# Optimization experiments

Hardware: AMD Instinct MI355X
Metric: run time of the kernel (lower is better)

The kernel has to match this reference:

```python
import jax, jax.numpy as jnp
import numpy as np

BT, H, V = 4096, 2048, 32000
BETA = 0.5
TEMPERATURE = 1.0
W_SCALE = 0.02  # keep logits in a sane range so softmax is not saturated


def setup_inputs() -> dict:
    key = jax.random.key(0)
    k1, k2, k3, k4 = jax.random.split(key, 4)
    return {
        "student_input": jax.random.normal(k1, (BT, H), dtype=jnp.float32),
        "teacher_input": jax.random.normal(k2, (BT, H), dtype=jnp.float32),
        "w_student": jax.random.normal(k3, (V, H), dtype=jnp.float32) * W_SCALE,
        "w_teacher": jax.random.normal(k4, (V, H), dtype=jnp.float32) * W_SCALE,
    }


def reference(student_input, teacher_input, w_student, w_teacher):
    # Fused linear + generalized Jensen-Shannon divergence (Liger semantics).
    # logits = x @ W.T, temperature-scaled before softmax.
    s_logits = jnp.einsum("nh,vh->nv", student_input, w_student) / TEMPERATURE
    t_logits = jnp.einsum("nh,vh->nv", teacher_input, w_teacher) / TEMPERATURE
    log_q = jax.nn.log_softmax(s_logits, axis=-1)  # student
    log_p = jax.nn.log_softmax(t_logits, axis=-1)  # teacher
    p = jnp.exp(log_p)
    q = jnp.exp(log_q)
    m = BETA * p + (1.0 - BETA) * q
    log_m = jnp.log(m)
    # JSD_beta(P || Q) = beta*KL(P||M) + (1-beta)*KL(Q||M), mean over tokens
    loss = BETA * jnp.sum(p * (log_p - log_m)) + (1.0 - BETA) * jnp.sum(q * (log_q - log_m))
    return loss / BT
```

## Files before the change

kernel.cpp:

```cpp
#include <hip/hip_runtime.h>
#include <cstdint>

#define BT 4096
#define HD 2048
#define VD 32000

typedef __attribute__((ext_vector_type(4))) float float4_t;
typedef __attribute__((ext_vector_type(4))) short short4_t;
typedef __attribute__((ext_vector_type(8))) short short8_t;
typedef __attribute__((ext_vector_type(8))) unsigned short ushort8_t;

constexpr int BM = 128, BN = 128, BK = 32;

__device__ __forceinline__ unsigned short f2bf(float f) {
  unsigned u = __float_as_uint(f);
  u += 0x7FFFu + ((u >> 16) & 1u);
  return (unsigned short)(u >> 16);
}

__device__ __forceinline__ float bf2f(unsigned short h) {
  return __uint_as_float((unsigned)h << 16);
}

__device__ __forceinline__ short8_t pack8(float4_t a, float4_t b) {
  short8_t h;
  h[0] = (short)f2bf(a.x); h[1] = (short)f2bf(a.y);
  h[2] = (short)f2bf(a.z); h[3] = (short)f2bf(a.w);
  h[4] = (short)f2bf(b.x); h[5] = (short)f2bf(b.y);
  h[6] = (short)f2bf(b.z); h[7] = (short)f2bf(b.w);
  return h;
}

__device__ __forceinline__ void async_copy16(const void* g, void* l) {
  __builtin_amdgcn_global_load_lds(
      (__attribute__((address_space(1))) void*)(uintptr_t)(g),
      (__attribute__((address_space(3))) void*)(uint32_t)(uintptr_t)(l),
      16, 0, 0);
}

__global__ __launch_bounds__(256) void cast_f32_to_bf16(
    const float4_t* __restrict__ in, short4_t* __restrict__ out, int n4) {
  for (int i = blockIdx.x * 256 + threadIdx.x; i < n4; i += gridDim.x * 256) {
    float4_t v = in[i];
    short4_t o;
    o.x = (short)f2bf(v.x); o.y = (short)f2bf(v.y);
    o.z = (short)f2bf(v.z); o.w = (short)f2bf(v.w);
    out[i] = o;
  }
}

__global__ __launch_bounds__(256) void cast_all_fp8(
    const float4_t* __restrict__ xs, const float4_t* __restrict__ xt,
    const float4_t* __restrict__ ws, const float4_t* __restrict__ wt,
    unsigned int* __restrict__ oxs, unsigned int* __restrict__ oxt,
    unsigned int* __restrict__ ows, unsigned int* __restrict__ owt,
    float* __restrict__ out) {
  const long XN4 = (long)BT * HD / 4;
  const long WN4 = (long)VD * HD / 4;
  const long total = 2 * (XN4 + WN4);
  const long i0 = blockIdx.x * 256L + threadIdx.x;
  if (i0 == 0) out[0] = 0.6931471805599453f;
  for (long i = i0; i < total; i += gridDim.x * 256L) {
    const float4_t* s; unsigned int* d; float scl; long j = i;
    if (j < XN4) { s = xs; d = oxs; scl = 1.f; }
    else if ((j -= XN4) < XN4) { s = xt; d = oxt; scl = 1.f; }
    else if ((j -= XN4) < WN4) { s = ws; d = ows; scl = 64.f; }
    else { j -= WN4; s = wt; d = owt; scl = 64.f; }
    float4_t v = s[j];
    int p = __builtin_amdgcn_cvt_pk_fp8_f32(v.x * scl, v.y * scl, 0, false);
    p = __builtin_amdgcn_cvt_pk_fp8_f32(v.z * scl, v.w * scl, p, true);
    d[j] = (unsigned int)p;
  }
}

__device__ __forceinline__ int swz(int row) { return (row ^ (row >> 2)) & 3; }

template <bool F32SRC>
__device__ __forceinline__ void ktile(const void* A, const void* B,
                                      float4_t (&acc)[4][4],
                                      unsigned short* As, unsigned short* Bs,
                                      int m0, int n0) {
  const int tid = threadIdx.x;
  const int lane = tid & 63;
  const int wave = tid >> 6;
  const int wm = wave >> 1, wn = wave & 1;
  const int r0 = tid >> 2, c0 = tid & 3;
  const int cg = c0 ^ swz(r0);
  const int row16 = lane & 15, kq = lane >> 4;
  const int kqs = kq ^ swz(row16);
  const int aoff = (wm * 64 + row16) * BK + kqs * 8;
  const int boff = (wn * 64 + row16) * BK + kqs * 8;
  const int lds0 = __builtin_amdgcn_readfirstlane(wave * 1024);
  const int lds1 = __builtin_amdgcn_readfirstlane(4096 + wave * 1024);

  const unsigned short* Ab = nullptr; const unsigned short* Bb = nullptr;
  const float* Af = nullptr; const float* Bf = nullptr;
  if constexpr (!F32SRC) {
    Ab = (const unsigned short*)A + (size_t)(m0 + r0) * HD + cg * 8;
    Bb = (const unsigned short*)B + (size_t)(n0 + r0) * HD + cg * 8;
  } else {
    Af = (const float*)A + (size_t)(m0 + r0) * HD + cg * 8;
    Bf = (const float*)B + (size_t)(n0 + r0) * HD + cg * 8;
  }

  for (int kb = 0; kb < HD / BK; ++kb) {
    const int ke = kb * BK;
    if constexpr (!F32SRC) {
      async_copy16(Ab + ke, (char*)As + lds0);
      async_copy16(Ab + (size_t)64 * HD + ke, (char*)As + lds1);
      async_copy16(Bb + ke, (char*)Bs + lds0);
      async_copy16(Bb + (size_t)64 * HD + ke, (char*)Bs + lds1);
    } else {
      short8_t hA0 = pack8(*(const float4_t*)(Af + ke), *(const float4_t*)(Af + ke + 4));
      short8_t hA1 = pack8(*(const float4_t*)(Af + (size_t)64 * HD + ke),
                           *(const float4_t*)(Af + (size_t)64 * HD + ke + 4));
      short8_t hB0 = pack8(*(const float4_t*)(Bf + ke), *(const float4_t*)(Bf + ke + 4));
      short8_t hB1 = pack8(*(const float4_t*)(Bf + (size_t)64 * HD + ke),
                           *(const float4_t*)(Bf + (size_t)64 * HD + ke + 4));
      *(short8_t*)((char*)As + tid * 16) = hA0;
      *(short8_t*)((char*)As + 4096 + tid * 16) = hA1;
      *(short8_t*)((char*)Bs + tid * 16) = hB0;
      *(short8_t*)((char*)Bs + 4096 + tid * 16) = hB1;
    }
    __syncthreads();
    short8_t af[4], bfv[4];
#pragma unroll
    for (int mi = 0; mi < 4; ++mi) af[mi] = *(const short8_t*)(As + aoff + mi * 16 * BK);
#pragma unroll
    for (int ni = 0; ni < 4; ++ni) bfv[ni] = *(const short8_t*)(Bs + boff + ni * 16 * BK);
#pragma unroll
    for (int mi = 0; mi < 4; ++mi)
#pragma unroll
      for (int ni = 0; ni < 4; ++ni)
        acc[mi][ni] = __builtin_amdgcn_mfma_f32_16x16x32_bf16(af[mi], bfv[ni], acc[mi][ni], 0, 0, 0);
    __syncthreads();
  }
}

template <bool F32SRC, bool STORE>
__global__ __launch_bounds__(256, 2) void gemm_pass1(
    const void* A0, const void* A1, const void* B0, const void* B1,
    float* __restrict__ rowsum, unsigned short* __restrict__ store) {
  __shared__ __align__(16) unsigned short As[BM * BK];
  __shared__ __align__(16) unsigned short Bs[BN * BK];
  const int m0 = blockIdx.x * BM;
  const int n0 = blockIdx.y * BN;
  const int z = blockIdx.z;
  const void* A = z ? A1 : A0;
  const void* B = z ? B1 : B0;
  float4_t acc[4][4] = {};
  ktile<F32SRC>(A, B, acc, As, Bs, m0, n0);

  const int tid = threadIdx.x;
  const int lane = tid & 63;
  const int wave = tid >> 6;
  const int wm = wave >> 1, wn = wave & 1;
  const int row16 = lane & 15, kq = lane >> 4;

  if constexpr (STORE) {
    unsigned short* st = store + (size_t)z * BT * VD;
#pragma unroll
    for (int mi = 0; mi < 4; ++mi)
#pragma unroll
      for (int r = 0; r < 4; ++r) {
        const size_t grow = (size_t)(m0 + wm * 64 + mi * 16 + kq * 4 + r);
        const size_t gc0 = (size_t)(n0 + wn * 64 + row16);
#pragma unroll
        for (int ni = 0; ni < 4; ++ni)
          st[grow * VD + gc0 + ni * 16] = f2bf(acc[mi][ni][r]);
      }
  }

  float* rs = rowsum + z * BT;
#pragma unroll
  for (int mi = 0; mi < 4; ++mi)
#pragma unroll
    for (int r = 0; r < 4; ++r) {
      float s = __expf(acc[mi][0][r]) + __expf(acc[mi][1][r]) +
                __expf(acc[mi][2][r]) + __expf(acc[mi][3][r]);
      s += __shfl_xor(s, 1);
      s += __shfl_xor(s, 2);
      s += __shfl_xor(s, 4);
      s += __shfl_xor(s, 8);
      if (row16 == 0) atomicAdd(&rs[m0 + wm * 64 + mi * 16 + kq * 4 + r], s);
    }
}

constexpr int NKT8 = HD / 64;

__global__ __launch_bounds__(512, 2) void gemm256_fp8_pass1(
    const unsigned char* __restrict__ fXs, const unsigned char* __restrict__ fXt,
    const unsigned char* __restrict__ fWs, const unsigned char* __restrict__ fWt,
    float* __restrict__ rowsum, unsigned short* __restrict__ store) {
  __shared__ __align__(16) unsigned char lds8[4 * 32768];

  const int z = blockIdx.y;
  const unsigned char* A = z ? fXt : fXs;
  const unsigned char* B = z ? fWt : fWs;

  const int o = blockIdx.x;
  const int s = (o & 7) * 250 + (o >> 3);
  const int m0 = (s & 15) * 256;
  const int n0 = (s >> 4) * 256;

  const int tid = threadIdx.x;
  const int lane = tid & 63;
  const int wave = tid >> 6;
  const int wm = wave >> 2;
  const int wn = wave & 3;
  const int row16 = lane & 15, kq = lane >> 4;
  const int rh = row16 >> 1;
  const int slot = row16 & 1;
  const int cA8 = (((slot << 2) | (kq >> 1)) ^ rh);

  const int lr = lane >> 3, lc = lane & 7;
  const int cl = lc ^ lr;
  const int k16 = (cl & 3) * 16;
  const int mloc0 = (wave * 2 + 0) * 16 + 2 * lr + (cl >> 2);
  const int mloc1 = (wave * 2 + 1) * 16 + 2 * lr + (cl >> 2);
  const unsigned char* srcA0 = A + (size_t)(m0 + mloc0) * HD + k16;
  const unsigned char* srcA1 = A + (size_t)(m0 + mloc1) * HD + k16;
  const unsigned char* srcB0 = B + (size_t)(n0 + mloc0) * HD + k16;
  const unsigned char* srcB1 = B + (size_t)(n0 + mloc1) * HD + k16;
  const int stA0 = __builtin_amdgcn_readfirstlane((wave * 2 + 0) * 1024);
  const int stA1 = __builtin_amdgcn_readfirstlane((wave * 2 + 1) * 1024);

#define STAGE(ktv, sl)                                                   \
  do {                                                                   \
    char* _sb = (char*)lds8 + (sl) * 32768;                              \
    async_copy16(srcA0 + (size_t)(ktv) * 64, _sb + stA0);                \
    async_copy16(srcA1 + (size_t)(ktv) * 64, _sb + stA1);                \
    async_copy16(srcB0 + (size_t)(ktv) * 64, _sb + 16384 + stA0);        \
    async_copy16(srcB1 + (size_t)(ktv) * 64, _sb + 16384 + stA1);        \
  } while (0)

  STAGE(0, 0);
  STAGE(1, 1);
  STAGE(2, 2);
  asm volatile("s_waitcnt vmcnt(8)" ::: "memory");
  __builtin_amdgcn_s_barrier();

  float4_t acc[8][4] = {};
  const int aoff0 = (wm * 64 + rh) * 128 + cA8 * 16 + (kq & 1) * 8;
  const int aoff1 = aoff0 ^ 32;
  const int boff0 = (wn * 32 + rh) * 128 + cA8 * 16 + (kq & 1) * 8;
  const int boff1 = boff0 ^ 32;

#pragma unroll 1
  for (int kt = 0; kt < NKT8; ++kt) {
    __builtin_amdgcn_sched_barrier(0);
    const int ktS = (kt + 3 > NKT8 - 1) ? NKT8 - 1 : kt + 3;
    STAGE(ktS, ktS & 3);

    const unsigned char* Asl = lds8 + (kt & 3) * 32768;
    const unsigned char* Bsl = Asl + 16384;
    long a0[8], a1[8], b0[4], b1[4];
#pragma unroll
    for (int mi = 0; mi < 8; ++mi) {
      a0[mi] = *(const long*)(Asl + aoff0 + mi * 1024);
      a1[mi] = *(const long*)(Asl + aoff1 + mi * 1024);
    }
#pragma unroll
    for (int ni = 0; ni < 4; ++ni) {
      b0[ni] = *(const long*)(Bsl + boff0 + ni * 1024);
      b1[ni] = *(const long*)(Bsl + boff1 + ni * 1024);
    }

    __builtin_amdgcn_s_setprio(1);
#pragma unroll
    for (int mi = 0; mi < 8; ++mi)
#pragma unroll
      for (int ni = 0; ni < 4; ++ni)
        acc[mi][ni] = __builtin_amdgcn_mfma_f32_16x16x32_fp8_fp8(a0[mi], b0[ni], acc[mi][ni], 0, 0, 0);
#pragma unroll
    for (int mi = 0; mi < 8; ++mi)
#pragma unroll
      for (int ni = 0; ni < 4; ++ni)
        acc[mi][ni] = __builtin_amdgcn_mfma_f32_16x16x32_fp8_fp8(a1[mi], b1[ni], acc[mi][ni], 0, 0, 0);
    __builtin_amdgcn_s_setprio(0);

    asm volatile("s_waitcnt vmcnt(8)" ::: "memory");
    __builtin_amdgcn_s_barrier();
  }
#undef STAGE

  asm volatile("s_waitcnt vmcnt(0)" ::: "memory");

  const float SCL = 0.015625f;
  unsigned short* st = store + (size_t)z * BT * VD;
  float* rs = rowsum + z * BT;
#pragma unroll
  for (int mi = 0; mi < 8; ++mi)
#pragma unroll
    for (int r = 0; r < 4; ++r) {
      const size_t grow = (size_t)(m0 + wm * 128 + mi * 16 + kq * 4 + r);
      const size_t gc0 = (size_t)(n0 + wn * 64 + row16);
      float zv[4];
#pragma unroll
      for (int ni = 0; ni < 4; ++ni) {
        zv[ni] = acc[mi][ni][r] * SCL;
        st[grow * VD + gc0 + ni * 16] = f2bf(zv[ni]);
      }
      float ssum = __expf(zv[0]) + __expf(zv[1]) + __expf(zv[2]) + __expf(zv[3]);
      ssum += __shfl_xor(ssum, 1);
      ssum += __shfl_xor(ssum, 2);
      ssum += __shfl_xor(ssum, 4);
      ssum += __shfl_xor(ssum, 8);
      if (row16 == 0) atomicAdd(&rs[grow], ssum);
    }
}

__global__ __launch_bounds__(256) void lse_fix(float* __restrict__ stats,
                                               float* __restrict__ out) {
  const int i = blockIdx.x * 256 + threadIdx.x;
  if (i < 2 * BT) stats[i] = __logf(stats[i]);
  if (i == 0) out[0] = 0.6931471805599453f;
}

__global__ void seed_out(float* __restrict__ out) {
  out[0] = 0.6931471805599453f;
}

__global__ __launch_bounds__(256) void loss_from_blogits(
    const ushort8_t* __restrict__ zs, const ushort8_t* __restrict__ zt,
    const float* __restrict__ rs, float* __restrict__ out) {
  const int row = blockIdx.x;
  const float es = __logf(rs[row]), et = __logf(rs[BT + row]);
  const ushort8_t* ps = zs + (size_t)row * (VD / 8);
  const ushort8_t* pt = zt + (size_t)row * (VD / 8);
  float local = 0.f;
  for (int i = threadIdx.x; i < VD / 8; i += 256) {
    const ushort8_t a = ps[i], b = pt[i];
#pragma unroll
    for (int c = 0; c < 8; ++c) {
      const float ls = bf2f(a[c]) - es, lt = bf2f(b[c]) - et;
      const float p = __expf(ls), q = __expf(lt);
      local += p * ls + q * lt - (p + q) * __logf(p + q);
    }
  }
  local += __shfl_xor(local, 1);
  local += __shfl_xor(local, 2);
  local += __shfl_xor(local, 4);
  local += __shfl_xor(local, 8);
  local += __shfl_xor(local, 16);
  local += __shfl_xor(local, 32);
  __shared__ float red[4];
  const int lane = threadIdx.x & 63, wave = threadIdx.x >> 6;
  if (lane == 0) red[wave] = local;
  __syncthreads();
  if (threadIdx.x == 0)
    atomicAdd(out, (red[0] + red[1] + red[2] + red[3]) * (0.5f / BT));
}

template <bool F32SRC>
__global__ __launch_bounds__(256, 2) void gemm_loss(
    const void* Asg, const void* Bsg, const void* Atg, const void* Btg,
    const float* __restrict__ lse, float* __restrict__ out) {
  __shared__ __align__(16) unsigned short As[BM * BK];
  __shared__ __align__(16) unsigned short Bs[BN * BK];
  __shared__ float red[4];
  const int m0 = blockIdx.x * BM;
  const int n0 = blockIdx.y * BN;
  float4_t acc_s[4][4] = {};
  ktile<F32SRC>(Asg, Bsg, acc_s, As, Bs, m0, n0);
  float4_t acc_t[4][4] = {};
  ktile<F32SRC>(Atg, Btg, acc_t, As, Bs, m0, n0);

  const int tid = threadIdx.x;
  const int lane = tid & 63;
  const int wave = tid >> 6;
  const int wm = wave >> 1;
  const int kq = lane >> 4;

  float local = 0.f;
#pragma unroll
  for (int mi = 0; mi < 4; ++mi)
#pragma unroll
    for (int r = 0; r < 4; ++r) {
      const int grow = m0 + wm * 64 + mi * 16 + kq * 4 + r;
      const float es = lse[grow], et = lse[BT + grow];
#pragma unroll
      for (int ni = 0; ni < 4; ++ni) {
        const float ls = acc_s[mi][ni][r] - es;
        const float lt = acc_t[mi][ni][r] - et;
        const float p = __expf(ls), q = __expf(lt);
        local += p * ls + q * lt - (p + q) * __logf(p + q);
      }
    }
  local += __shfl_xor(local, 1);
  local += __shfl_xor(local, 2);
  local += __shfl_xor(local, 4);
  local += __shfl_xor(local, 8);
  local += __shfl_xor(local, 16);
  local += __shfl_xor(local, 32);
  if (lane == 0) red[wave] = local;
  __syncthreads();
  if (tid == 0) atomicAdd(out, (red[0] + red[1] + red[2] + red[3]) * (0.5f / BT));
}

extern "C" void kernel_launch(void* const* d_in, const int* in_sizes, int n_in,
                              void* d_out, int out_size, void* d_ws, size_t ws_size,
                              hipStream_t stream) {
  const float* Xs = (const float*)d_in[0];
  const float* Xt = (const float*)d_in[1];
  const float* Ws = (const float*)d_in[2];
  const float* Wt = (const float*)d_in[3];
  float* out = (float*)d_out;
  char* ws = (char*)d_ws;

  const size_t STATS_B = (size_t)2 * BT * sizeof(float);
  const size_t XB8 = (size_t)BT * HD;
  const size_t WB8 = (size_t)VD * HD;
  const size_t XB = (size_t)BT * HD * 2;
  const size_t WB = (size_t)VD * HD * 2;
  const size_t LOGIT_B = (size_t)2 * BT * VD * 2;
  const size_t FP8_NEED = STATS_B + 2 * XB8 + 2 * WB8 + LOGIT_B;
  const size_t PRECAST_NEED = STATS_B + 2 * XB + 2 * WB;
  const size_t MID_NEED = STATS_B + LOGIT_B;

  float* stats = (float*)ws;
  hipMemsetAsync(stats, 0, STATS_B, stream);

  const dim3 blk(256);
  const dim3 g1(BT / BM, VD / BN, 2);
  const dim3 g2(BT / BM, VD / BN, 1);
  const int XN4 = BT * HD / 4;
  const int WN4 = VD * HD / 4;

  if (ws_size >= FP8_NEED) {
    unsigned char* fXs = (unsigned char*)(ws + STATS_B);
    unsigned char* fXt = fXs + XB8;
    unsigned char* fWs = fXt + XB8;
    unsigned char* fWt = fWs + WB8;
    unsigned short* logits = (unsigned short*)(ws + STATS_B + 2 * XB8 + 2 * WB8);
    cast_all_fp8<<<dim3(2048), blk, 0, stream>>>(
        (const float4_t*)Xs, (const float4_t*)Xt,
        (const float4_t*)Ws, (const float4_t*)Wt,
        (unsigned int*)fXs, (unsigned int*)fXt,
        (unsigned int*)fWs, (unsigned int*)fWt, out);
    gemm256_fp8_pass1<<<dim3((BT / 256) * (VD / 256), 2), dim3(512), 0, stream>>>(
        fXs, fXt, fWs, fWt, stats, logits);
    loss_from_blogits<<<dim3(BT), blk, 0, stream>>>(
        (const ushort8_t*)logits,
        (const ushort8_t*)(logits + (size_t)BT * VD), stats, out);
  } else if (ws_size >= MID_NEED) {
    unsigned short* logits = (unsigned short*)(ws + STATS_B);
    gemm_pass1<true, true><<<g1, blk, 0, stream>>>(Xs, Xt, Ws, Wt, stats, logits);
    seed_out<<<dim3(1), dim3(1), 0, stream>>>(out);
    loss_from_blogits<<<dim3(BT), blk, 0, stream>>>(
        (const ushort8_t*)logits,
        (const ushort8_t*)(logits + (size_t)BT * VD), stats, out);
  } else if (ws_size >= PRECAST_NEED) {
    unsigned short* bXs = (unsigned short*)(ws + STATS_B);
    unsigned short* bXt = bXs + (size_t)BT * HD;
    unsigned short* bWs = bXt + (size_t)BT * HD;
    unsigned short* bWt = bWs + (size_t)VD * HD;
    cast_f32_to_bf16<<<dim3(512), blk, 0, stream>>>((const float4_t*)Xs, (short4_t*)bXs, XN4);
    cast_f32_to_bf16<<<dim3(512), blk, 0, stream>>>((const float4_t*)Xt, (short4_t*)bXt, XN4);
    cast_f32_to_bf16<<<dim3(2048), blk, 0, stream>>>((const float4_t*)Ws, (short4_t*)bWs, WN4);
    cast_f32_to_bf16<<<dim3(2048), blk, 0, stream>>>((const float4_t*)Wt, (short4_t*)bWt, WN4);
    gemm_pass1<false, false><<<g1, blk, 0, stream>>>(bXs, bXt, bWs, bWt, stats, nullptr);
    lse_fix<<<dim3(32), blk, 0, stream>>>(stats, out);
    gemm_loss<false><<<g2, blk, 0, stream>>>(bXs, bWs, bXt, bWt, stats, out);
  } else {
    gemm_pass1<true, false><<<g1, blk, 0, stream>>>(Xs, Xt, Ws, Wt, stats, nullptr);
    lse_fix<<<dim3(32), blk, 0, stream>>>(stats, out);
    gemm_loss<true><<<g2, blk, 0, stream>>>(Xs, Ws, Xt, Wt, stats, out);
  }
  (void)in_sizes; (void)n_in; (void)out_size;
}
```

Measured before the change: 1.575 ms.

## Interleave fp8 cast layout so GEMM reads 16-byte LDS fragments

The fp8 cast kernel now writes each 64-byte K chunk in a permuted order: every thread packs 16 values from two 8-float runs 32 elements apart into one 16-byte store. This lets the GEMM inner loop fetch both K-halves of each MFMA operand with a single 128-bit LDS read instead of two 64-bit reads, halving LDS load instructions. The cast also issues wider global stores. The change relies on the cast permutation and the GEMM swizzle offsets matching exactly, which is the correctness risk.

```diff
diff --git a/kernel.cpp b/kernel.cpp
--- a/kernel.cpp
+++ b/kernel.cpp
@@ -9,6 +9,8 @@
 typedef __attribute__((ext_vector_type(4))) short short4_t;
 typedef __attribute__((ext_vector_type(8))) short short8_t;
 typedef __attribute__((ext_vector_type(8))) unsigned short ushort8_t;
+typedef __attribute__((ext_vector_type(2))) long long2_t;
+typedef __attribute__((ext_vector_type(4))) unsigned int uint4_t;
 
 constexpr int BM = 128, BN = 128, BK = 32;
 
@@ -49,27 +51,40 @@
   }
 }
 
-__global__ __launch_bounds__(256) void cast_all_fp8(
-    const float4_t* __restrict__ xs, const float4_t* __restrict__ xt,
-    const float4_t* __restrict__ ws, const float4_t* __restrict__ wt,
-    unsigned int* __restrict__ oxs, unsigned int* __restrict__ oxt,
-    unsigned int* __restrict__ ows, unsigned int* __restrict__ owt,
+__device__ __forceinline__ unsigned int pk_fp8x4(float a, float b, float c, float d) {
+  int p = __builtin_amdgcn_cvt_pk_fp8_f32(a, b, 0, false);
+  p = __builtin_amdgcn_cvt_pk_fp8_f32(c, d, p, true);
+  return (unsigned int)p;
+}
+
+__global__ __launch_bounds__(256) void cast_all_fp8i(
+    const float* __restrict__ xs, const float* __restrict__ xt,
+    const float* __restrict__ ws, const float* __restrict__ wt,
+    uint4_t* __restrict__ oxs, uint4_t* __restrict__ oxt,
+    uint4_t* __restrict__ ows, uint4_t* __restrict__ owt,
     float* __restrict__ out) {
-  const long XN4 = (long)BT * HD / 4;
-  const long WN4 = (long)VD * HD / 4;
-  const long total = 2 * (XN4 + WN4);
+  const long XP = (long)BT * HD / 16;
+  const long WP = (long)VD * HD / 16;
+  const long total = 2 * (XP + WP);
   const long i0 = blockIdx.x * 256L + threadIdx.x;
   if (i0 == 0) out[0] = 0.6931471805599453f;
   for (long i = i0; i < total; i += gridDim.x * 256L) {
-    const float4_t* s; unsigned int* d; float scl; long j = i;
-    if (j < XN4) { s = xs; d = oxs; scl = 1.f; }
-    else if ((j -= XN4) < XN4) { s = xt; d = oxt; scl = 1.f; }
-    else if ((j -= XN4) < WN4) { s = ws; d = ows; scl = 64.f; }
-    else { j -= WN4; s = wt; d = owt; scl = 64.f; }
-    float4_t v = s[j];
-    int p = __builtin_amdgcn_cvt_pk_fp8_f32(v.x * scl, v.y * scl, 0, false);
-    p = __builtin_amdgcn_cvt_pk_fp8_f32(v.z * scl, v.w * scl, p, true);
-    d[j] = (unsigned int)p;
+    const float* s; uint4_t* d; float scl; long j = i;
+    if (j < XP) { s = xs; d = oxs; scl = 1.f; }
+    else if ((j -= XP) < XP) { s = xt; d = oxt; scl = 1.f; }
+    else if ((j -= XP) < WP) { s = ws; d = ows; scl = 64.f; }
+    else { j -= WP; s = wt; d = owt; scl = 64.f; }
+    const float* sp = s + ((j >> 2) * 64 + (j & 3) * 8);
+    float4_t v0 = *(const float4_t*)(sp);
+    float4_t v1 = *(const float4_t*)(sp + 4);
+    float4_t v2 = *(const float4_t*)(sp + 32);
+    float4_t v3 = *(const float4_t*)(sp + 36);
+    uint4_t o;
+    o.x = pk_fp8x4(v0.x * scl, v0.y * scl, v0.z * scl, v0.w * scl);
+    o.y = pk_fp8x4(v1.x * scl, v1.y * scl, v1.z * scl, v1.w * scl);
+    o.z = pk_fp8x4(v2.x * scl, v2.y * scl, v2.z * scl, v2.w * scl);
+    o.w = pk_fp8x4(v3.x * scl, v3.y * scl, v3.z * scl, v3.w * scl);
+    d[j] = o;
   }
 }
 
@@ -210,8 +225,7 @@
   const int wn = wave & 3;
   const int row16 = lane & 15, kq = lane >> 4;
   const int rh = row16 >> 1;
-  const int slot = row16 & 1;
-  const int cA8 = (((slot << 2) | (kq >> 1)) ^ rh);
+  const int cA = (((row16 & 1) << 2) | kq) ^ rh;
 
   const int lr = lane >> 3, lc = lane & 7;
   const int cl = lc ^ lr;
@@ -241,10 +255,8 @@
   __builtin_amdgcn_s_barrier();
 
   float4_t acc[8][4] = {};
-  const int aoff0 = (wm * 64 + rh) * 128 + cA8 * 16 + (kq & 1) * 8;
-  const int aoff1 = aoff0 ^ 32;
-  const int boff0 = (wn * 32 + rh) * 128 + cA8 * 16 + (kq & 1) * 8;
-  const int boff1 = boff0 ^ 32;
+  const int aoff = (wm * 64 + rh) * 128 + cA * 16;
+  const int boff = (wn * 32 + rh) * 128 + cA * 16;
 
 #pragma unroll 1
   for (int kt = 0; kt < NKT8; ++kt) {
@@ -254,29 +266,23 @@
 
     const unsigned char* Asl = lds8 + (kt & 3) * 32768;
     const unsigned char* Bsl = Asl + 16384;
-    long a0[8], a1[8], b0[4], b1[4];
-#pragma unroll
-    for (int mi = 0; mi < 8; ++mi) {
-      a0[mi] = *(const long*)(Asl + aoff0 + mi * 1024);
-      a1[mi] = *(const long*)(Asl + aoff1 + mi * 1024);
-    }
-#pragma unroll
-    for (int ni = 0; ni < 4; ++ni) {
-      b0[ni] = *(const long*)(Bsl + boff0 + ni * 1024);
-      b1[ni] = *(const long*)(Bsl + boff1 + ni * 1024);
-    }
+    long2_t a[8], b[4];
+#pragma unroll
+    for (int mi = 0; mi < 8; ++mi) a[mi] = *(const long2_t*)(Asl + aoff + mi * 1024);
+#pragma unroll
+    for (int ni = 0; ni < 4; ++ni) b[ni] = *(const long2_t*)(Bsl + boff + ni * 1024);
 
     __builtin_amdgcn_s_setprio(1);
 #pragma unroll
     for (int mi = 0; mi < 8; ++mi)
 #pragma unroll
       for (int ni = 0; ni < 4; ++ni)
-        acc[mi][ni] = __builtin_amdgcn_mfma_f32_16x16x32_fp8_fp8(a0[mi], b0[ni], acc[mi][ni], 0, 0, 0);
+        acc[mi][ni] = __builtin_amdgcn_mfma_f32_16x16x32_fp8_fp8(a[mi].x, b[ni].x, acc[mi][ni], 0, 0, 0);
 #pragma unroll
     for (int mi = 0; mi < 8; ++mi)
 #pragma unroll
       for (int ni = 0; ni < 4; ++ni)
-        acc[mi][ni] = __builtin_amdgcn_mfma_f32_16x16x32_fp8_fp8(a1[mi], b1[ni], acc[mi][ni], 0, 0, 0);
+        acc[mi][ni] = __builtin_amdgcn_mfma_f32_16x16x32_fp8_fp8(a[mi].y, b[ni].y, acc[mi][ni], 0, 0, 0);
     __builtin_amdgcn_s_setprio(0);
 
     asm volatile("s_waitcnt vmcnt(8)" ::: "memory");
@@ -433,11 +439,9 @@
     unsigned char* fWs = fXt + XB8;
     unsigned char* fWt = fWs + WB8;
     unsigned short* logits = (unsigned short*)(ws + STATS_B + 2 * XB8 + 2 * WB8);
-    cast_all_fp8<<<dim3(2048), blk, 0, stream>>>(
-        (const float4_t*)Xs, (const float4_t*)Xt,
-        (const float4_t*)Ws, (const float4_t*)Wt,
-        (unsigned int*)fXs, (unsigned int*)fXt,
-        (unsigned int*)fWs, (unsigned int*)fWt, out);
+    cast_all_fp8i<<<dim3(2048), blk, 0, stream>>>(
+        Xs, Xt, Ws, Wt,
+        (uint4_t*)fXs, (uint4_t*)fXt, (uint4_t*)fWs, (uint4_t*)fWt, out);
     gemm256_fp8_pass1<<<dim3((BT / 256) * (VD / 256), 2), dim3(512), 0, stream>>>(
         fXs, fXt, fWs, fWt, stats, logits);
     loss_from_blogits<<<dim3(BT), blk, 0, stream>>>(
```

New measurement: 1.437 ms. -8.7%, faster.
